# Optimization experiments

Measured on AMD Instinct MI355X. Metric: run time of the kernel, lower is better.

## Reference

```python
import jax, jax.numpy as jnp
import numpy as np

NEG_SLOPE = 0.2

def _gat_conv(x, src, dst, W, att_src, att_dst, bias, num_nodes):
    # x: [N, Fin], W: [H*C, Fin], att_*: [H, C], bias: [H*C]
    H, C = att_src.shape
    xh = (x @ W.T).reshape(num_nodes, H, C)            # [N,H,C]
    a_s = jnp.einsum('nhc,hc->nh', xh, att_src)         # [N,H]
    a_d = jnp.einsum('nhc,hc->nh', xh, att_dst)
    e = jax.nn.leaky_relu(a_s[src] + a_d[dst], NEG_SLOPE)  # [E,H]
    # segment softmax over destination node per head
    m = jax.ops.segment_max(e, dst, num_segments=num_nodes)      # [N,H]
    ex = jnp.exp(e - m[dst])
    s = jax.ops.segment_sum(ex, dst, num_segments=num_nodes)     # [N,H]
    alpha = ex / (s[dst] + 1e-16)                                # [E,H]
    msg = xh[src] * alpha[:, :, None]                            # [E,H,C]
    out = jax.ops.segment_sum(msg, dst, num_segments=num_nodes)  # [N,H,C]
    return out.reshape(num_nodes, H * C) + bias


def setup_inputs() -> dict:
    key = jax.random.key(0)
    ks = jax.random.split(key, 16)
    N, E, Fin, Hd, H1, G = 50000, 800000, 128, 128, 4, 128
    x = jax.random.normal(ks[0], (N, Fin), dtype=jnp.float32)
    edge_index = jax.random.randint(ks[1], (2, E), 0, N, dtype=jnp.int64)
    batch = jnp.sort(jax.random.randint(ks[2], (N,), 0, G, dtype=jnp.int64))
    sc1 = 1.0 / np.sqrt(Fin)
    sc2 = 1.0 / np.sqrt(Hd * H1)
    sch = 1.0 / np.sqrt(Hd)
    return {
        'x': x, 'edge_index': edge_index, 'batch': batch,
        'W1': jax.random.normal(ks[3], (Hd * H1, Fin), dtype=jnp.float32) * sc1,
        'as1': jax.random.normal(ks[4], (H1, Hd), dtype=jnp.float32) * 0.1,
        'ad1': jax.random.normal(ks[5], (H1, Hd), dtype=jnp.float32) * 0.1,
        'b1': jnp.zeros((Hd * H1,), dtype=jnp.float32),
        'W2': jax.random.normal(ks[6], (Hd, Hd * H1), dtype=jnp.float32) * sc2,
        'as2': jax.random.normal(ks[7], (1, Hd), dtype=jnp.float32) * 0.1,
        'ad2': jax.random.normal(ks[8], (1, Hd), dtype=jnp.float32) * 0.1,
        'b2': jnp.zeros((Hd,), dtype=jnp.float32),
        'Wh1': jax.random.normal(ks[9], (Hd, Hd), dtype=jnp.float32) * sch,
        'bh1': jnp.zeros((Hd,), dtype=jnp.float32),
        'Wh2': jax.random.normal(ks[10], (1, Hd), dtype=jnp.float32) * sch,
        'bh2': jnp.zeros((1,), dtype=jnp.float32),
    }


def reference(x, edge_index, batch, W1, as1, ad1, b1, W2, as2, ad2, b2, Wh1, bh1, Wh2, bh2):
    N = x.shape[0]
    G = 128  # num graphs
    # add self loops (PyG GATConv default)
    loops = jnp.arange(N, dtype=edge_index.dtype)
    src = jnp.concatenate([edge_index[0], loops])
    dst = jnp.concatenate([edge_index[1], loops])
    h = _gat_conv(x, src, dst, W1, as1, ad1, b1, N)   # [N, 512]
    h = jax.nn.elu(h)
    h = _gat_conv(h, src, dst, W2, as2, ad2, b2, N)   # [N, 128]
    h = jax.nn.elu(h)
    # global mean pool over batch
    sums = jax.ops.segment_sum(h, batch, num_segments=G)
    cnts = jax.ops.segment_sum(jnp.ones((N,), dtype=h.dtype), batch, num_segments=G)
    pooled = sums / jnp.maximum(cnts, 1.0)[:, None]   # [G, 128]
    z = jax.nn.relu(pooled @ Wh1.T + bh1)
    out = z @ Wh2.T + bh2                             # [G, 1]
    return out.reshape(-1)
```

## Files before the change

kernel.cpp:

```cpp
#include <hip/hip_runtime.h>
#include <cstdint>
#include <cstddef>

#define NEG_SLOPE 0.2f

typedef _Float16 f16x8 __attribute__((ext_vector_type(8)));
typedef _Float16 f16x2 __attribute__((ext_vector_type(2)));
typedef float    f32x4 __attribute__((ext_vector_type(4)));
typedef float    f32x2 __attribute__((ext_vector_type(2)));

__device__ __forceinline__ float leaky(float x){ return x > 0.f ? x : NEG_SLOPE * x; }
__device__ __forceinline__ float elu(float x){ return x > 0.f ? x : __expf(x) - 1.f; }

__global__ __launch_bounds__(256) void k_front(const float* __restrict__ W1,
                                               const float* __restrict__ W2,
                                               const float* __restrict__ as1,
                                               const float* __restrict__ ad1,
                                               _Float16* __restrict__ W1hi, _Float16* __restrict__ W1lo,
                                               _Float16* __restrict__ W2hi, _Float16* __restrict__ W2lo,
                                               float* __restrict__ w_s, float* __restrict__ w_d,
                                               const int* __restrict__ ei, int* __restrict__ deg,
                                               unsigned short* __restrict__ rank,
                                               const int* __restrict__ batch, int* __restrict__ gstart,
                                               int E, int Ep, int N, int G, int nbc)
{
    int b = blockIdx.x;
    if (b < 512) {
        const float* src = (b < 256) ? W1 : W2;
        _Float16* hi = (b < 256) ? W1hi : W2hi;
        _Float16* lo = (b < 256) ? W1lo : W2lo;
        int i = ((b & 255) << 8) + threadIdx.x;
        float v = src[i];
        _Float16 h = (_Float16)v;
        hi[i] = h;
        lo[i] = (_Float16)(v - (float)h);
    } else if (b < 514) {
        int h = (b - 512) * 2 + (threadIdx.x >> 7);
        int k = threadIdx.x & 127;
        float s = 0.f, d = 0.f;
        for (int c = 0; c < 128; ++c) {
            float w = W1[((size_t)(h * 128 + c)) * 128 + k];
            s += as1[h * 128 + c] * w;
            d += ad1[h * 128 + c] * w;
        }
        w_s[h * 128 + k] = s;
        w_d[h * 128 + k] = d;
    } else if (b < 514 + nbc) {
        int e = (b - 514) * 256 + threadIdx.x;
        if (e >= Ep) return;
        int dst = (e < E) ? ei[E + e] : (e - E);
        rank[e] = (unsigned short)atomicAdd(&deg[dst], 1);
    } else {
        int n = (b - 514 - nbc) * 256 + threadIdx.x;
        if (n >= N) return;
        int bb = batch[n];
        int prev = (n == 0) ? -1 : batch[n - 1];
        for (int g = prev + 1; g <= bb; ++g) gstart[g] = n;
        if (n == N - 1)
            for (int g = bb + 1; g <= G; ++g) gstart[g] = N;
    }
}

__global__ __launch_bounds__(1024) void k_scan_attn(const int* __restrict__ deg,
                                                    int* __restrict__ start,
                                                    int* __restrict__ sums,
                                                    int Ntot, int N, int nscan,
                                                    const float* __restrict__ x,
                                                    const float* __restrict__ w_s,
                                                    const float* __restrict__ w_d,
                                                    float* __restrict__ a_s,
                                                    float* __restrict__ a_d,
                                                    _Float16* __restrict__ xh)
{
    if ((int)blockIdx.x < nscan) {
        __shared__ int sm[1024];
        int tid = threadIdx.x;
        int i = blockIdx.x * 1024 + tid;
        int v = (i < N) ? deg[i] : 0;
        sm[tid] = v; __syncthreads();
        for (int off = 1; off < 1024; off <<= 1) {
            int t = (tid >= off) ? sm[tid - off] : 0;
            __syncthreads();
            sm[tid] += t;
            __syncthreads();
        }
        if (i < Ntot) start[i] = sm[tid] - v;
        if (tid == 1023) sums[blockIdx.x] = sm[1023];
    } else {
        int n = (blockIdx.x - nscan) * 16 + (threadIdx.x >> 6);
        if (n >= N) return;
        int lane = threadIdx.x & 63;
        float2 xv = *(const float2*)(x + (size_t)n * 128 + lane * 2);
        f16x2 hv = { (_Float16)xv.x, (_Float16)xv.y };
        *(f16x2*)(xh + (size_t)n * 128 + lane * 2) = hv;
        float ps[4], pd[4];
        #pragma unroll
        for (int h = 0; h < 4; ++h) {
            float2 sv = *(const float2*)(w_s + h * 128 + lane * 2);
            float2 dv = *(const float2*)(w_d + h * 128 + lane * 2);
            ps[h] = xv.x * sv.x + xv.y * sv.y;
            pd[h] = xv.x * dv.x + xv.y * dv.y;
        }
        #pragma unroll
        for (int h = 0; h < 4; ++h)
            for (int off = 32; off; off >>= 1) {
                ps[h] += __shfl_xor(ps[h], off);
                pd[h] += __shfl_xor(pd[h], off);
            }
        if (lane == 0) {
            *(float4*)(a_s + (size_t)n * 4) = make_float4(ps[0], ps[1], ps[2], ps[3]);
            *(float4*)(a_d + (size_t)n * 4) = make_float4(pd[0], pd[1], pd[2], pd[3]);
        }
    }
}

__global__ __launch_bounds__(1024) void k_scanC(int* __restrict__ start,
                                                const int* __restrict__ sums, int Ntot)
{
    int add = 0;
    for (int b = 0; b < (int)blockIdx.x; ++b) add += sums[b];
    int i = blockIdx.x * 1024 + threadIdx.x;
    if (i < Ntot) start[i] += add;
}

__global__ void k_fill(const int* __restrict__ ei, const int* __restrict__ start,
                       const unsigned short* __restrict__ rank,
                       unsigned short* __restrict__ csr_src, int E, int Ep)
{
    int e = blockIdx.x * blockDim.x + threadIdx.x;
    if (e >= Ep) return;
    int src, dst;
    if (e < E) { src = ei[e]; dst = ei[E + e]; } else { src = dst = e - E; }
    csr_src[start[dst] + rank[e]] = (unsigned short)src;
}

#define LSG 40
#define CP  136
__global__ __launch_bounds__(256, 2) void k_gemm12(
    const _Float16* __restrict__ agg,
    const _Float16* __restrict__ W1hi, const _Float16* __restrict__ W1lo,
    const float* __restrict__ b1,
    const _Float16* __restrict__ W2hi, const _Float16* __restrict__ W2lo,
    _Float16* __restrict__ xh2,
    const float* __restrict__ as2, const float* __restrict__ ad2,
    float* __restrict__ As2, float* __restrict__ Ad2, int M)
{
    __shared__ __align__(16) _Float16 smem[128 * LSG * 3 + 128 * CP];
    _Float16* As  = smem;
    _Float16* Bhs = smem + 128 * LSG;
    _Float16* Bls = smem + 256 * LSG;
    _Float16* Ct  = smem + 384 * LSG;

    const int tid = threadIdx.x;
    const int wave = tid >> 6, lane = tid & 63;
    const int wm = wave >> 1, wn = wave & 1;
    const int quad = lane >> 4, l16 = lane & 15;
    const int m0 = blockIdx.x * 128;

    f32x4 acc2[4][4] = {};

    for (int h = 0; h < 4; ++h) {
        f32x4 acc1[4][4] = {};
        for (int k0 = 0; k0 < 128; k0 += 32) {
            #pragma unroll
            for (int q = 0; q < 2; ++q) {
                int idx = tid + q * 256;
                int row = idx >> 2, kq = idx & 3;
                int rg = m0 + row;
                f16x8 va = {};
                if (rg < M) va = *(const f16x8*)(agg + (size_t)rg * 512 + h * 128 + k0 + kq * 8);
                *(f16x8*)&As[row * LSG + kq * 8] = va;
                size_t brow = (size_t)(h * 128 + row) * 128 + k0 + kq * 8;
                *(f16x8*)&Bhs[row * LSG + kq * 8] = *(const f16x8*)(W1hi + brow);
                *(f16x8*)&Bls[row * LSG + kq * 8] = *(const f16x8*)(W1lo + brow);
            }
            __syncthreads();
            f16x8 af[4], bhf[4], blf[4];
            #pragma unroll
            for (int i = 0; i < 4; ++i) {
                af[i]  = *(const f16x8*)&As [(wm * 64 + i * 16 + l16) * LSG + quad * 8];
                bhf[i] = *(const f16x8*)&Bhs[(wn * 64 + i * 16 + l16) * LSG + quad * 8];
                blf[i] = *(const f16x8*)&Bls[(wn * 64 + i * 16 + l16) * LSG + quad * 8];
            }
            #pragma unroll
            for (int i = 0; i < 4; ++i)
                #pragma unroll
                for (int j = 0; j < 4; ++j) {
                    acc1[i][j] = __builtin_amdgcn_mfma_f32_16x16x32_f16(af[i], bhf[j], acc1[i][j], 0, 0, 0);
                    acc1[i][j] = __builtin_amdgcn_mfma_f32_16x16x32_f16(af[i], blf[j], acc1[i][j], 0, 0, 0);
                }
            __syncthreads();
        }
        #pragma unroll
        for (int j = 0; j < 4; ++j) {
            int n = wn * 64 + j * 16 + l16;
            float bb = b1[h * 128 + n];
            #pragma unroll
            for (int i = 0; i < 4; ++i)
                #pragma unroll
                for (int r = 0; r < 4; ++r)
                    Ct[(wm * 64 + i * 16 + quad * 4 + r) * CP + n] = (_Float16)elu(acc1[i][j][r] + bb);
        }
        __syncthreads();
        for (int k0 = 0; k0 < 128; k0 += 32) {
            #pragma unroll
            for (int q = 0; q < 2; ++q) {
                int idx = tid + q * 256;
                int row = idx >> 2, kq = idx & 3;
                size_t brow = (size_t)row * 512 + h * 128 + k0 + kq * 8;
                *(f16x8*)&Bhs[row * LSG + kq * 8] = *(const f16x8*)(W2hi + brow);
                *(f16x8*)&Bls[row * LSG + kq * 8] = *(const f16x8*)(W2lo + brow);
            }
            __syncthreads();
            f16x8 af[4], bhf[4], blf[4];
            #pragma unroll
            for (int i = 0; i < 4; ++i) {
                af[i]  = *(const f16x8*)&Ct [(wm * 64 + i * 16 + l16) * CP + k0 + quad * 8];
                bhf[i] = *(const f16x8*)&Bhs[(wn * 64 + i * 16 + l16) * LSG + quad * 8];
                blf[i] = *(const f16x8*)&Bls[(wn * 64 + i * 16 + l16) * LSG + quad * 8];
            }
            #pragma unroll
            for (int i = 0; i < 4; ++i)
                #pragma unroll
                for (int j = 0; j < 4; ++j) {
                    acc2[i][j] = __builtin_amdgcn_mfma_f32_16x16x32_f16(af[i], bhf[j], acc2[i][j], 0, 0, 0);
                    acc2[i][j] = __builtin_amdgcn_mfma_f32_16x16x32_f16(af[i], blf[j], acc2[i][j], 0, 0, 0);
                }
            __syncthreads();
        }
    }

    #pragma unroll
    for (int j = 0; j < 4; ++j) {
        int n = wn * 64 + j * 16 + l16;
        #pragma unroll
        for (int i = 0; i < 4; ++i)
            #pragma unroll
            for (int r = 0; r < 4; ++r)
                Ct[(wm * 64 + i * 16 + quad * 4 + r) * CP + n] = (_Float16)acc2[i][j][r];
    }
    __syncthreads();
    for (int c = tid; c < 2048; c += 256) {
        int row = c >> 4, col8 = (c & 15) * 8;
        int m = m0 + row;
        if (m < M)
            *(f16x8*)(xh2 + (size_t)m * 128 + col8) = *(const f16x8*)&Ct[row * CP + col8];
    }
    {
        int row = tid >> 1, half = tid & 1;
        int d = m0 + row;
        float ss = 0.f, sd = 0.f;
        const _Float16* rp = &Ct[row * CP + half * 64];
        #pragma unroll
        for (int c8 = 0; c8 < 8; ++c8) {
            f16x8 v = *(const f16x8*)(rp + c8 * 8);
            #pragma unroll
            for (int c = 0; c < 8; ++c) {
                float f = (float)v[c];
                int n = half * 64 + c8 * 8 + c;
                ss += f * as2[n];
                sd += f * ad2[n];
            }
        }
        ss += __shfl_xor(ss, 1);
        sd += __shfl_xor(sd, 1);
        if (half == 0 && d < M) { As2[d] = ss; Ad2[d] = sd; }
    }
}

__global__ __launch_bounds__(256) void k_gat1(const int* __restrict__ start,
                                              const unsigned short* __restrict__ csr,
                                              const float* __restrict__ a_s,
                                              const float* __restrict__ a_d,
                                              const _Float16* __restrict__ x,
                                              _Float16* __restrict__ agg, int N)
{
    int d = blockIdx.x * 16 + (threadIdx.x >> 4);
    if (d >= N) return;
    int g16 = threadIdx.x & 15;
    int beg = start[d], end = start[d + 1];
    int deg = end - beg;
    float4 ad4 = *(const float4*)(a_d + (size_t)d * 4);

    float sum0 = 0.f, sum1 = 0.f, sum2 = 0.f, sum3 = 0.f;
    f32x2 acc[4][4] = {};
    const _Float16* xb = x + g16 * 8;

    for (int base = 0; base < deg; base += 16) {
        int nch = deg - base; if (nch > 16) nch = 16;
        int s = 0;
        float e0 = 0.f, e1 = 0.f, e2 = 0.f, e3 = 0.f;
        if (g16 < nch) {
            s = csr[beg + base + g16];
            float4 as4 = *(const float4*)(a_s + (size_t)s * 4);
            e0 = __expf(leaky(as4.x + ad4.x));
            e1 = __expf(leaky(as4.y + ad4.y));
            e2 = __expf(leaky(as4.z + ad4.z));
            e3 = __expf(leaky(as4.w + ad4.w));
            sum0 += e0; sum1 += e1; sum2 += e2; sum3 += e3;
        }
        int t = 0;
        for (; t + 8 <= nch; t += 8) {
            int si[8];
            #pragma unroll
            for (int u = 0; u < 8; ++u) si[u] = __shfl(s, t + u, 16);
            f16x8 hv[8];
            #pragma unroll
            for (int u = 0; u < 8; ++u) hv[u] = *(const f16x8*)(xb + (size_t)si[u] * 128);
            #pragma unroll
            for (int u = 0; u < 8; ++u) {
                float w0 = __shfl(e0, t + u, 16), w1 = __shfl(e1, t + u, 16);
                float w2 = __shfl(e2, t + u, 16), w3 = __shfl(e3, t + u, 16);
                #pragma unroll
                for (int p = 0; p < 4; ++p) {
                    f32x2 v = { (float)hv[u][2*p], (float)hv[u][2*p+1] };
                    acc[0][p] += w0 * v;
                    acc[1][p] += w1 * v;
                    acc[2][p] += w2 * v;
                    acc[3][p] += w3 * v;
                }
            }
        }
        for (; t + 4 <= nch; t += 4) {
            int sA = __shfl(s, t, 16),     sB = __shfl(s, t + 1, 16);
            int sC = __shfl(s, t + 2, 16), sD = __shfl(s, t + 3, 16);
            f16x8 hA = *(const f16x8*)(xb + (size_t)sA * 128);
            f16x8 hB = *(const f16x8*)(xb + (size_t)sB * 128);
            f16x8 hC = *(const f16x8*)(xb + (size_t)sC * 128);
            f16x8 hD = *(const f16x8*)(xb + (size_t)sD * 128);
            float w0A = __shfl(e0, t, 16),     w1A = __shfl(e1, t, 16);
            float w2A = __shfl(e2, t, 16),     w3A = __shfl(e3, t, 16);
            float w0B = __shfl(e0, t + 1, 16), w1B = __shfl(e1, t + 1, 16);
            float w2B = __shfl(e2, t + 1, 16), w3B = __shfl(e3, t + 1, 16);
            float w0C = __shfl(e0, t + 2, 16), w1C = __shfl(e1, t + 2, 16);
            float w2C = __shfl(e2, t + 2, 16), w3C = __shfl(e3, t + 2, 16);
            float w0D = __shfl(e0, t + 3, 16), w1D = __shfl(e1, t + 3, 16);
            float w2D = __shfl(e2, t + 3, 16), w3D = __shfl(e3, t + 3, 16);
            #pragma unroll
            for (int p = 0; p < 4; ++p) {
                f32x2 vA = { (float)hA[2*p], (float)hA[2*p+1] };
                f32x2 vB = { (float)hB[2*p], (float)hB[2*p+1] };
                f32x2 vC = { (float)hC[2*p], (float)hC[2*p+1] };
                f32x2 vD = { (float)hD[2*p], (float)hD[2*p+1] };
                acc[0][p] += w0A * vA + w0B * vB + w0C * vC + w0D * vD;
                acc[1][p] += w1A * vA + w1B * vB + w1C * vC + w1D * vD;
                acc[2][p] += w2A * vA + w2B * vB + w2C * vC + w2D * vD;
                acc[3][p] += w3A * vA + w3B * vB + w3C * vC + w3D * vD;
            }
        }
        for (; t < nch; ++t) {
            int   si = __shfl(s,  t, 16);
            float w0 = __shfl(e0, t, 16);
            float w1 = __shfl(e1, t, 16);
            float w2 = __shfl(e2, t, 16);
            float w3 = __shfl(e3, t, 16);
            f16x8 hv = *(const f16x8*)(xb + (size_t)si * 128);
            #pragma unroll
            for (int p = 0; p < 4; ++p) {
                f32x2 v = { (float)hv[2*p], (float)hv[2*p+1] };
                acc[0][p] += w0 * v;
                acc[1][p] += w1 * v;
                acc[2][p] += w2 * v;
                acc[3][p] += w3 * v;
            }
        }
    }
    #pragma unroll
    for (int o = 1; o < 16; o <<= 1) {
        sum0 += __shfl_xor(sum0, o, 16); sum1 += __shfl_xor(sum1, o, 16);
        sum2 += __shfl_xor(sum2, o, 16); sum3 += __shfl_xor(sum3, o, 16);
    }
    float inv[4] = { 1.f / (sum0 + 1e-16f), 1.f / (sum1 + 1e-16f),
                     1.f / (sum2 + 1e-16f), 1.f / (sum3 + 1e-16f) };
    _Float16* o = agg + (size_t)d * 512 + g16 * 8;
    #pragma unroll
    for (int h = 0; h < 4; ++h) {
        f16x8 ov;
        #pragma unroll
        for (int p = 0; p < 4; ++p) {
            ov[2 * p]     = (_Float16)(acc[h][p].x * inv[h]);
            ov[2 * p + 1] = (_Float16)(acc[h][p].y * inv[h]);
        }
        *(f16x8*)(o + h * 128) = ov;
    }
}

__global__ __launch_bounds__(256) void k_gat2(const int* __restrict__ start,
                                              const unsigned short* __restrict__ csr,
                                              const float* __restrict__ a_s,
                                              const float* __restrict__ a_d,
                                              const _Float16* __restrict__ xh2,
                                              const float* __restrict__ b2,
                                              _Float16* __restrict__ h2, int N)
{
    int d = blockIdx.x * 16 + (threadIdx.x >> 4);
    if (d >= N) return;
    int g16 = threadIdx.x & 15;
    int beg = start[d], end = start[d + 1];
    int deg = end - beg;
    float ad = a_d[d];

    float sum = 0.f;
    f32x2 acc[4] = {};
    const _Float16* xb = xh2 + g16 * 8;

    for (int base = 0; base < deg; base += 16) {
        int nch = deg - base; if (nch > 16) nch = 16;
        int s = 0; float e = 0.f;
        if (g16 < nch) {
            s = csr[beg + base + g16];
            e = __expf(leaky(a_s[s] + ad));
            sum += e;
        }
        int t = 0;
        for (; t + 8 <= nch; t += 8) {
            int si[8];
            #pragma unroll
            for (int u = 0; u < 8; ++u) si[u] = __shfl(s, t + u, 16);
            f16x8 hv[8];
            #pragma unroll
            for (int u = 0; u < 8; ++u) hv[u] = *(const f16x8*)(xb + (size_t)si[u] * 128);
            #pragma unroll
            for (int u = 0; u < 8; ++u) {
                float w = __shfl(e, t + u, 16);
                #pragma unroll
                for (int p = 0; p < 4; ++p) {
                    f32x2 v = { (float)hv[u][2*p], (float)hv[u][2*p+1] };
                    acc[p] += w * v;
                }
            }
        }
        for (; t + 4 <= nch; t += 4) {
            int sA = __shfl(s, t, 16),     sB = __shfl(s, t + 1, 16);
            int sC = __shfl(s, t + 2, 16), sD = __shfl(s, t + 3, 16);
            f16x8 hA = *(const f16x8*)(xb + (size_t)sA * 128);
            f16x8 hB = *(const f16x8*)(xb + (size_t)sB * 128);
            f16x8 hC = *(const f16x8*)(xb + (size_t)sC * 128);
            f16x8 hD = *(const f16x8*)(xb + (size_t)sD * 128);
            float wA = __shfl(e, t, 16),     wB = __shfl(e, t + 1, 16);
            float wC = __shfl(e, t + 2, 16), wD = __shfl(e, t + 3, 16);
            #pragma unroll
            for (int p = 0; p < 4; ++p) {
                f32x2 vA = { (float)hA[2*p], (float)hA[2*p+1] };
                f32x2 vB = { (float)hB[2*p], (float)hB[2*p+1] };
                f32x2 vC = { (float)hC[2*p], (float)hC[2*p+1] };
                f32x2 vD = { (float)hD[2*p], (float)hD[2*p+1] };
                acc[p] += wA * vA + wB * vB + wC * vC + wD * vD;
            }
        }
        for (; t < nch; ++t) {
            int   si = __shfl(s, t, 16);
            float w  = __shfl(e, t, 16);
            f16x8 hv = *(const f16x8*)(xb + (size_t)si * 128);
            #pragma unroll
            for (int p = 0; p < 4; ++p) {
                f32x2 v = { (float)hv[2*p], (float)hv[2*p+1] };
                acc[p] += w * v;
            }
        }
    }
    #pragma unroll
    for (int o = 1; o < 16; o <<= 1) sum += __shfl_xor(sum, o, 16);
    float inv = 1.f / (sum + 1e-16f);
    f16x8 ov;
    #pragma unroll
    for (int p = 0; p < 4; ++p) {
        ov[2 * p]     = (_Float16)elu(acc[p].x * inv + b2[g16 * 8 + 2 * p]);
        ov[2 * p + 1] = (_Float16)elu(acc[p].y * inv + b2[g16 * 8 + 2 * p + 1]);
    }
    *(f16x8*)(h2 + (size_t)d * 128 + g16 * 8) = ov;
}

#define PCH 64
__global__ __launch_bounds__(128) void k_poolA(const _Float16* __restrict__ h2,
                                               const int* __restrict__ batch,
                                               float* __restrict__ pooled, int N)
{
    int c = threadIdx.x;
    int n0 = blockIdx.x * PCH;
    int n1 = n0 + PCH < N ? n0 + PCH : N;
    if (n0 >= N) return;
    int g = batch[n0];
    float acc = 0.f;
    for (int n = n0; n < n1; ++n) {
        int bg = batch[n];
        if (bg != g) { atomicAdd(&pooled[(size_t)g * 128 + c], acc); acc = 0.f; g = bg; }
        acc += (float)h2[(size_t)n * 128 + c];
    }
    atomicAdd(&pooled[(size_t)g * 128 + c], acc);
}

__global__ __launch_bounds__(128) void k_head(const float* __restrict__ pooled,
                                              const int* __restrict__ gstart,
                                              const float* __restrict__ Wh1,
                                              const float* __restrict__ bh1,
                                              const float* __restrict__ Wh2,
                                              const float* __restrict__ bh2,
                                              float* __restrict__ out)
{
    int g = blockIdx.x, c = threadIdx.x;
    __shared__ float p[128];
    __shared__ float red[128];
    float cf = (float)(gstart[g + 1] - gstart[g]); cf = cf > 1.f ? cf : 1.f;
    p[c] = pooled[(size_t)g * 128 + c] / cf;
    __syncthreads();
    float z = bh1[c];
    for (int k = 0; k < 128; ++k) z += p[k] * Wh1[c * 128 + k];
    z = z > 0.f ? z : 0.f;
    red[c] = z * Wh2[c];
    __syncthreads();
    for (int st = 64; st > 0; st >>= 1) { if (c < st) red[c] += red[c + st]; __syncthreads(); }
    if (c == 0) out[g] = red[0] + bh2[0];
}

extern "C" void kernel_launch(void* const* d_in, const int* in_sizes, int n_in,
                              void* d_out, int out_size, void* d_ws, size_t ws_size,
                              hipStream_t stream)
{
    const float* x   = (const float*)d_in[0];
    const int*   ei  = (const int*)d_in[1];
    const int*   bat = (const int*)d_in[2];
    const float* W1  = (const float*)d_in[3];
    const float* as1 = (const float*)d_in[4];
    const float* ad1 = (const float*)d_in[5];
    const float* b1  = (const float*)d_in[6];
    const float* W2  = (const float*)d_in[7];
    const float* as2 = (const float*)d_in[8];
    const float* ad2 = (const float*)d_in[9];
    const float* b2  = (const float*)d_in[10];
    const float* Wh1 = (const float*)d_in[11];
    const float* bh1 = (const float*)d_in[12];
    const float* Wh2 = (const float*)d_in[13];
    const float* bh2 = (const float*)d_in[14];
    float* out = (float*)d_out;

    const int N  = in_sizes[0] / 128;
    const int E  = in_sizes[1] / 2;
    const int Ep = E + N;
    const int G  = 128;
    const int nscan = (N + 1 + 1023) / 1024;

    char* w = (char*)d_ws;
    size_t off = 0;
    auto alloc = [&](size_t bytes) -> char* {
        char* p = w + off; off += (bytes + 511) & ~(size_t)511; return p;
    };
    _Float16* x_h  = (_Float16*)alloc((size_t)N * 128 * 2);
    _Float16* agg  = (_Float16*)alloc((size_t)N * 512 * 2);
    _Float16* xh2h = (_Float16*)alloc((size_t)N * 128 * 2);
    _Float16* h2   = (_Float16*)alloc((size_t)N * 128 * 2);
    float*    As1  = (float*)alloc((size_t)N * 4 * 4);
    float*    Ad1  = (float*)alloc((size_t)N * 4 * 4);
    float*    As2  = (float*)alloc((size_t)N * 4);
    float*    Ad2  = (float*)alloc((size_t)N * 4);
    float*    w_s1 = (float*)alloc(512 * 4);
    float*    w_d1 = (float*)alloc(512 * 4);
    _Float16* W1hi = (_Float16*)alloc(65536 * 2);
    _Float16* W1lo = (_Float16*)alloc(65536 * 2);
    _Float16* W2hi = (_Float16*)alloc(65536 * 2);
    _Float16* W2lo = (_Float16*)alloc(65536 * 2);
    int* startb = (int*)alloc((size_t)(N + 1) * 4);
    unsigned short* csr  = (unsigned short*)alloc((size_t)Ep * 2);
    unsigned short* rank = (unsigned short*)alloc((size_t)Ep * 2);
    int* sums   = (int*)alloc(4096);
    int* gstart = (int*)alloc((size_t)(G + 1) * 4);
    char* zbase = w + off;
    int*   deg    = (int*)alloc((size_t)N * 4);
    float* pooled = (float*)alloc((size_t)G * 128 * 4);
    size_t zbytes = (size_t)((w + off) - zbase);

    hipMemsetAsync(zbase, 0, zbytes, stream);

    int nbc = (Ep + 255) / 256, nbg = (N + 255) / 256;
    k_front<<<514 + nbc + nbg, 256, 0, stream>>>(W1, W2, as1, ad1, W1hi, W1lo, W2hi, W2lo,
                                                 w_s1, w_d1, ei, deg, rank, bat, gstart,
                                                 E, Ep, N, G, nbc);
    k_scan_attn<<<nscan + (N + 15) / 16, 1024, 0, stream>>>(deg, startb, sums, N + 1, N, nscan,
                                                            x, w_s1, w_d1, As1, Ad1, x_h);
    k_scanC<<<nscan, 1024, 0, stream>>>(startb, sums, N + 1);
    k_fill<<<(Ep + 255) / 256, 256, 0, stream>>>(ei, startb, rank, csr, E, Ep);
    k_gat1<<<(N + 15) / 16, 256, 0, stream>>>(startb, csr, As1, Ad1, x_h, agg, N);
    k_gemm12<<<(N + 127) / 128, 256, 0, stream>>>(agg, W1hi, W1lo, b1, W2hi, W2lo,
                                                  xh2h, as2, ad2, As2, Ad2, N);
    k_gat2<<<(N + 15) / 16, 256, 0, stream>>>(startb, csr, As2, Ad2, xh2h, b2, h2, N);
    k_poolA<<<(N + PCH - 1) / PCH, 128, 0, stream>>>(h2, bat, pooled, N);
    k_head<<<G, 128, 0, stream>>>(pooled, gstart, Wh1, bh1, Wh2, bh2, out);
}
```

Before: 331.3 us.

## Halve gemm12 row tile to 64 and repack intermediate layout for occupancy

The fused two-layer GEMM kernel now processes 64 rows per block instead of 128. This halves the accumulator registers per wave, raises the launch-bounds occupancy hint from 2 to 3, and doubles the block count (about 782 blocks versus 391) so the GPU's compute units are better covered. The intermediate ELU tile is stored in a chunked [k-chunk][row][LSG] layout so shared memory shrinks, and the epilogue reuses the start of shared memory. The cost is that the W1/W2 hi/lo weight tiles are reloaded twice as often per output row, raising global and LDS traffic.

```diff
diff --git a/kernel.cpp b/kernel.cpp
--- a/kernel.cpp
+++ b/kernel.cpp
@@ -136,7 +136,7 @@
 
 #define LSG 40
 #define CP  136
-__global__ __launch_bounds__(256, 2) void k_gemm12(
+__global__ __launch_bounds__(256, 3) void k_gemm12(
     const _Float16* __restrict__ agg,
     const _Float16* __restrict__ W1hi, const _Float16* __restrict__ W1lo,
     const float* __restrict__ b1,
@@ -145,45 +145,50 @@
     const float* __restrict__ as2, const float* __restrict__ ad2,
     float* __restrict__ As2, float* __restrict__ Ad2, int M)
 {
-    __shared__ __align__(16) _Float16 smem[128 * LSG * 3 + 128 * CP];
+    __shared__ __align__(16) _Float16 smem[2560 + 5120 + 5120 + 10240];
     _Float16* As  = smem;
-    _Float16* Bhs = smem + 128 * LSG;
-    _Float16* Bls = smem + 256 * LSG;
-    _Float16* Ct  = smem + 384 * LSG;
+    _Float16* Bhs = smem + 2560;
+    _Float16* Bls = smem + 7680;
+    _Float16* Ct  = smem + 12800;
 
     const int tid = threadIdx.x;
     const int wave = tid >> 6, lane = tid & 63;
     const int wm = wave >> 1, wn = wave & 1;
     const int quad = lane >> 4, l16 = lane & 15;
-    const int m0 = blockIdx.x * 128;
-
-    f32x4 acc2[4][4] = {};
+    const int m0 = blockIdx.x * 64;
+
+    f32x4 acc2[2][4] = {};
 
     for (int h = 0; h < 4; ++h) {
-        f32x4 acc1[4][4] = {};
+        f32x4 acc1[2][4] = {};
         for (int k0 = 0; k0 < 128; k0 += 32) {
-            #pragma unroll
-            for (int q = 0; q < 2; ++q) {
-                int idx = tid + q * 256;
-                int row = idx >> 2, kq = idx & 3;
+            {
+                int row = tid >> 2, kq = tid & 3;
                 int rg = m0 + row;
                 f16x8 va = {};
                 if (rg < M) va = *(const f16x8*)(agg + (size_t)rg * 512 + h * 128 + k0 + kq * 8);
                 *(f16x8*)&As[row * LSG + kq * 8] = va;
+            }
+            #pragma unroll
+            for (int q = 0; q < 2; ++q) {
+                int idx = tid + q * 256;
+                int row = idx >> 2, kq = idx & 3;
                 size_t brow = (size_t)(h * 128 + row) * 128 + k0 + kq * 8;
                 *(f16x8*)&Bhs[row * LSG + kq * 8] = *(const f16x8*)(W1hi + brow);
                 *(f16x8*)&Bls[row * LSG + kq * 8] = *(const f16x8*)(W1lo + brow);
             }
             __syncthreads();
-            f16x8 af[4], bhf[4], blf[4];
-            #pragma unroll
-            for (int i = 0; i < 4; ++i) {
-                af[i]  = *(const f16x8*)&As [(wm * 64 + i * 16 + l16) * LSG + quad * 8];
-                bhf[i] = *(const f16x8*)&Bhs[(wn * 64 + i * 16 + l16) * LSG + quad * 8];
-                blf[i] = *(const f16x8*)&Bls[(wn * 64 + i * 16 + l16) * LSG + quad * 8];
-            }
-            #pragma unroll
-            for (int i = 0; i < 4; ++i)
+            f16x8 af[2], bhf[4], blf[4];
+            #pragma unroll
+            for (int i = 0; i < 2; ++i)
+                af[i]  = *(const f16x8*)&As [(wm * 32 + i * 16 + l16) * LSG + quad * 8];
+            #pragma unroll
+            for (int j = 0; j < 4; ++j) {
+                bhf[j] = *(const f16x8*)&Bhs[(wn * 64 + j * 16 + l16) * LSG + quad * 8];
+                blf[j] = *(const f16x8*)&Bls[(wn * 64 + j * 16 + l16) * LSG + quad * 8];
+            }
+            #pragma unroll
+            for (int i = 0; i < 2; ++i)
                 #pragma unroll
                 for (int j = 0; j < 4; ++j) {
                     acc1[i][j] = __builtin_amdgcn_mfma_f32_16x16x32_f16(af[i], bhf[j], acc1[i][j], 0, 0, 0);
@@ -194,12 +199,15 @@
         #pragma unroll
         for (int j = 0; j < 4; ++j) {
             int n = wn * 64 + j * 16 + l16;
+            int chunk = n >> 5, kin = n & 31;
             float bb = b1[h * 128 + n];
             #pragma unroll
-            for (int i = 0; i < 4; ++i)
+            for (int i = 0; i < 2; ++i)
                 #pragma unroll
-                for (int r = 0; r < 4; ++r)
-                    Ct[(wm * 64 + i * 16 + quad * 4 + r) * CP + n] = (_Float16)elu(acc1[i][j][r] + bb);
+                for (int r = 0; r < 4; ++r) {
+                    int row = wm * 32 + i * 16 + quad * 4 + r;
+                    Ct[(chunk * 64 + row) * LSG + kin] = (_Float16)elu(acc1[i][j][r] + bb);
+                }
         }
         __syncthreads();
         for (int k0 = 0; k0 < 128; k0 += 32) {
@@ -212,15 +220,17 @@
                 *(f16x8*)&Bls[row * LSG + kq * 8] = *(const f16x8*)(W2lo + brow);
             }
             __syncthreads();
-            f16x8 af[4], bhf[4], blf[4];
-            #pragma unroll
-            for (int i = 0; i < 4; ++i) {
-                af[i]  = *(const f16x8*)&Ct [(wm * 64 + i * 16 + l16) * CP + k0 + quad * 8];
-                bhf[i] = *(const f16x8*)&Bhs[(wn * 64 + i * 16 + l16) * LSG + quad * 8];
-                blf[i] = *(const f16x8*)&Bls[(wn * 64 + i * 16 + l16) * LSG + quad * 8];
-            }
-            #pragma unroll
-            for (int i = 0; i < 4; ++i)
+            f16x8 af[2], bhf[4], blf[4];
+            #pragma unroll
+            for (int i = 0; i < 2; ++i)
+                af[i]  = *(const f16x8*)&Ct[((k0 >> 5) * 64 + wm * 32 + i * 16 + l16) * LSG + quad * 8];
+            #pragma unroll
+            for (int j = 0; j < 4; ++j) {
+                bhf[j] = *(const f16x8*)&Bhs[(wn * 64 + j * 16 + l16) * LSG + quad * 8];
+                blf[j] = *(const f16x8*)&Bls[(wn * 64 + j * 16 + l16) * LSG + quad * 8];
+            }
+            #pragma unroll
+            for (int i = 0; i < 2; ++i)
                 #pragma unroll
                 for (int j = 0; j < 4; ++j) {
                     acc2[i][j] = __builtin_amdgcn_mfma_f32_16x16x32_f16(af[i], bhf[j], acc2[i][j], 0, 0, 0);
@@ -230,41 +240,42 @@
         }
     }
 
+    _Float16* Ep = smem;
     #pragma unroll
     for (int j = 0; j < 4; ++j) {
         int n = wn * 64 + j * 16 + l16;
         #pragma unroll
-        for (int i = 0; i < 4; ++i)
+        for (int i = 0; i < 2; ++i)
             #pragma unroll
             for (int r = 0; r < 4; ++r)
-                Ct[(wm * 64 + i * 16 + quad * 4 + r) * CP + n] = (_Float16)acc2[i][j][r];
+                Ep[(wm * 32 + i * 16 + quad * 4 + r) * CP + n] = (_Float16)acc2[i][j][r];
     }
     __syncthreads();
-    for (int c = tid; c < 2048; c += 256) {
+    for (int c = tid; c < 1024; c += 256) {
         int row = c >> 4, col8 = (c & 15) * 8;
         int m = m0 + row;
         if (m < M)
-            *(f16x8*)(xh2 + (size_t)m * 128 + col8) = *(const f16x8*)&Ct[row * CP + col8];
+            *(f16x8*)(xh2 + (size_t)m * 128 + col8) = *(const f16x8*)&Ep[row * CP + col8];
     }
     {
-        int row = tid >> 1, half = tid & 1;
+        int row = tid >> 2, qtr = tid & 3;
         int d = m0 + row;
         float ss = 0.f, sd = 0.f;
-        const _Float16* rp = &Ct[row * CP + half * 64];
+        const _Float16* rp = &Ep[row * CP + qtr * 32];
         #pragma unroll
-        for (int c8 = 0; c8 < 8; ++c8) {
+        for (int c8 = 0; c8 < 4; ++c8) {
             f16x8 v = *(const f16x8*)(rp + c8 * 8);
             #pragma unroll
             for (int c = 0; c < 8; ++c) {
                 float f = (float)v[c];
-                int n = half * 64 + c8 * 8 + c;
+                int n = qtr * 32 + c8 * 8 + c;
                 ss += f * as2[n];
                 sd += f * ad2[n];
             }
         }
-        ss += __shfl_xor(ss, 1);
-        sd += __shfl_xor(sd, 1);
-        if (half == 0 && d < M) { As2[d] = ss; Ad2[d] = sd; }
+        ss += __shfl_xor(ss, 1); sd += __shfl_xor(sd, 1);
+        ss += __shfl_xor(ss, 2); sd += __shfl_xor(sd, 2);
+        if (qtr == 0 && d < M) { As2[d] = ss; Ad2[d] = sd; }
     }
 }
 
@@ -580,8 +591,8 @@
     k_scanC<<<nscan, 1024, 0, stream>>>(startb, sums, N + 1);
     k_fill<<<(Ep + 255) / 256, 256, 0, stream>>>(ei, startb, rank, csr, E, Ep);
     k_gat1<<<(N + 15) / 16, 256, 0, stream>>>(startb, csr, As1, Ad1, x_h, agg, N);
-    k_gemm12<<<(N + 127) / 128, 256, 0, stream>>>(agg, W1hi, W1lo, b1, W2hi, W2lo,
-                                                  xh2h, as2, ad2, As2, Ad2, N);
+    k_gemm12<<<(N + 63) / 64, 256, 0, stream>>>(agg, W1hi, W1lo, b1, W2hi, W2lo,
+                                                xh2h, as2, ad2, As2, Ad2, N);
     k_gat2<<<(N + 15) / 16, 256, 0, stream>>>(startb, csr, As2, Ad2, xh2h, b2, h2, N);
     k_poolA<<<(N + PCH - 1) / PCH, 128, 0, stream>>>(h2, bat, pooled, N);
     k_head<<<G, 128, 0, stream>>>(pooled, gstart, Wh1, bh1, Wh2, bh2, out);
```

After: 348.9 us. +5.3%, slower.
